# Performance work log

Measured on AMD Instinct MI355X. Metric: run time of the kernel, lower is better.

Reference implementation:

```python
import jax, jax.numpy as jnp
import numpy as np


def conv(x, w, stride=1, pad=0):
    return jax.lax.conv_general_dilated(
        x, w, (stride, stride), [(pad, pad), (pad, pad)],
        dimension_numbers=('NCHW', 'OIHW', 'NCHW'))


def group_norm(x, scale, bias, groups=32, eps=1e-5):
    B, C, H, W = x.shape
    xg = x.reshape(B, groups, C // groups, H, W)
    m = xg.mean(axis=(2, 3, 4), keepdims=True)
    v = xg.var(axis=(2, 3, 4), keepdims=True)
    xn = ((xg - m) * jax.lax.rsqrt(v + eps)).reshape(B, C, H, W)
    return xn * scale[None, :, None, None] + bias[None, :, None, None]


def bilinear_sample(x, py, px):
    # x: [B,C,H,W]; py, px: [B,K,Ho,Wo] absolute sampling coords.
    # Returns [B,C,K,Ho,Wo]; out-of-bounds corners contribute zero
    # (matches deform-conv CUDA kernel semantics).
    B, C, H, W = x.shape
    y0 = jnp.floor(py)
    x0 = jnp.floor(px)
    wy1 = py - y0
    wx1 = px - x0
    xf = x.reshape(B, C, H * W)
    Ksp = py.shape[1:]

    def corner(yi, xi, wy, wx):
        valid = (yi >= 0) & (yi < H) & (xi >= 0) & (xi < W)
        yc = jnp.clip(yi, 0, H - 1).astype(jnp.int32)
        xc = jnp.clip(xi, 0, W - 1).astype(jnp.int32)
        idx = (yc * W + xc).reshape(B, 1, -1)          # [B,1,K*Ho*Wo]
        v = jnp.take_along_axis(xf, idx, axis=2).reshape(B, C, *Ksp)
        w = (wy * wx * valid).astype(x.dtype)[:, None]  # [B,1,K,Ho,Wo]
        return v * w

    return (corner(y0, x0, 1.0 - wy1, 1.0 - wx1)
            + corner(y0, x0 + 1, 1.0 - wy1, wx1)
            + corner(y0 + 1, x0, wy1, 1.0 - wx1)
            + corner(y0 + 1, x0 + 1, wy1, wx1))


def setup_inputs() -> dict:
    key = jax.random.key(0)
    ks = jax.random.split(key, 8)
    B, Cin, H, W = 4, 1024, 64, 64
    Cb = 256  # bottleneck channels
    x = jax.random.normal(ks[0], (B, Cin, H, W), dtype=jnp.float32)
    w1 = jax.random.normal(ks[1], (Cb, Cin, 1, 1), dtype=jnp.float32) * (1.0 / np.sqrt(Cin))
    w_off = jax.random.normal(ks[2], (27, Cb, 3, 3), dtype=jnp.float32) * 0.01
    b_off = jnp.zeros((27,), dtype=jnp.float32)
    w2 = jax.random.normal(ks[3], (Cb, Cb, 3, 3), dtype=jnp.float32) * (1.0 / np.sqrt(Cb * 9))
    w3 = jax.random.normal(ks[4], (Cin, Cb, 1, 1), dtype=jnp.float32) * (1.0 / np.sqrt(Cb))
    return {
        'x': x,
        'w1': w1, 'gn1_scale': jnp.ones((Cb,), jnp.float32), 'gn1_bias': jnp.zeros((Cb,), jnp.float32),
        'w_off': w_off, 'b_off': b_off,
        'w2': w2, 'gn2_scale': jnp.ones((Cb,), jnp.float32), 'gn2_bias': jnp.zeros((Cb,), jnp.float32),
        'w3': w3, 'gn3_scale': jnp.ones((Cin,), jnp.float32), 'gn3_bias': jnp.zeros((Cin,), jnp.float32),
        'stride': 4,
    }


def reference(x, w1, gn1_scale, gn1_bias, w_off, b_off, w2, gn2_scale, gn2_bias,
              w3, gn3_scale, gn3_bias, stride):
    # stride only selects the offset-conv / norm bank (single bank here).
    out = conv(x, w1)                                   # 1x1
    out = jax.nn.relu(group_norm(out, gn1_scale, gn1_bias))

    om = conv(out, w_off, pad=1) + b_off[None, :, None, None]  # [B,27,H,W]
    K = 9
    off_x = om[:, :K]
    off_y = om[:, K:2 * K]
    mask = jax.nn.sigmoid(om[:, 2 * K:])                # [B,9,H,W]

    B, C, H, W = out.shape
    ky, kx = jnp.meshgrid(jnp.arange(3), jnp.arange(3), indexing='ij')
    ky = (ky.reshape(K) - 1).astype(om.dtype)           # kernel taps, pad=1, dil=1
    kx = (kx.reshape(K) - 1).astype(om.dtype)
    grid_y = jnp.arange(H, dtype=om.dtype)[None, :, None] + ky[:, None, None]  # [9,H,1]
    grid_x = jnp.arange(W, dtype=om.dtype)[None, None, :] + kx[:, None, None]  # [9,1,W]
    py = grid_y[None] + off_y                           # [B,9,H,W]
    px = grid_x[None] + off_x

    sampled = bilinear_sample(out, py, px) * mask[:, None]      # [B,C,9,H,W]
    out = jnp.einsum('bckhw,ock->bohw', sampled, w2.reshape(w2.shape[0], w2.shape[1], K))
    out = jax.nn.relu(group_norm(out, gn2_scale, gn2_bias))

    out = conv(out, w3)                                 # 1x1
    out = group_norm(out, gn3_scale, gn3_bias)
    return jax.nn.relu(out + x)
```

## Files before the change

kernel.cpp:

```cpp
#include <hip/hip_runtime.h>
#include <math.h>

#define BATCH 4
#define CIN   1024
#define CB    256
#define HH    64
#define WW    64
#define PP    4096
#define EPSV  1e-5f

using shortx8 = __attribute__((ext_vector_type(8))) short;
using floatx4 = __attribute__((ext_vector_type(4))) float;
using intx4   = __attribute__((ext_vector_type(4))) int;

static __device__ inline unsigned short f2bf(float f) {
    unsigned int u = __float_as_uint(f);
    u += 0x7fffu + ((u >> 16) & 1u);
    return (unsigned short)(u >> 16);
}
static __device__ inline float bf2f(unsigned short s) {
    return __uint_as_float(((unsigned int)s) << 16);
}
static __device__ inline float bflo(unsigned int u) {
    return __uint_as_float(u << 16);
}
static __device__ inline float bfhi(unsigned int u) {
    return __uint_as_float(u & 0xffff0000u);
}

__global__ __launch_bounds__(256)
void gemm_bf16(const unsigned short* __restrict__ A,
               const unsigned short* __restrict__ BTg,
               float* __restrict__ Cg, int M, int N, int K) {
    const int b = blockIdx.z;
    const unsigned short* BT = BTg + (size_t)b * N * K;
    float* C = Cg + (size_t)b * M * N;
    const int m0 = blockIdx.y * 128;
    const int n0 = blockIdx.x * 128;
    const int tid = threadIdx.x;
    const int lane = tid & 63;
    const int wid = tid >> 6;
    const int l15 = lane & 15;
    const int quad = lane >> 4;

    __shared__ __align__(16) unsigned short As[128 * 40];
    __shared__ __align__(16) unsigned short Bs[128 * 40];

    floatx4 acc[2][8];
#pragma unroll
    for (int i = 0; i < 2; i++)
#pragma unroll
        for (int j = 0; j < 8; j++) acc[i][j] = (floatx4){0.f, 0.f, 0.f, 0.f};

    const int row = tid >> 1;
    const int half = tid & 1;

    for (int k0 = 0; k0 < K; k0 += 32) {
        const unsigned short* ga = A + (size_t)(m0 + row) * K + k0 + half * 16;
        const unsigned short* gb = BT + (size_t)(n0 + row) * K + k0 + half * 16;
        float4 a0 = *(const float4*)ga;
        float4 a1 = *(const float4*)(ga + 8);
        float4 b0 = *(const float4*)gb;
        float4 b1 = *(const float4*)(gb + 8);
        __syncthreads();
        *(float4*)((char*)As + row * 80 + half * 32) = a0;
        *(float4*)((char*)As + row * 80 + half * 32 + 16) = a1;
        *(float4*)((char*)Bs + row * 80 + half * 32) = b0;
        *(float4*)((char*)Bs + row * 80 + half * 32 + 16) = b1;
        __syncthreads();
        shortx8 af[2], bf[8];
#pragma unroll
        for (int i = 0; i < 2; i++)
            af[i] = *(const shortx8*)((const char*)As +
                    (wid * 32 + 16 * i + l15) * 80 + quad * 16);
#pragma unroll
        for (int j = 0; j < 8; j++)
            bf[j] = *(const shortx8*)((const char*)Bs +
                    (16 * j + l15) * 80 + quad * 16);
#pragma unroll
        for (int i = 0; i < 2; i++)
#pragma unroll
            for (int j = 0; j < 8; j++)
                acc[i][j] = __builtin_amdgcn_mfma_f32_16x16x32_bf16(
                    af[i], bf[j], acc[i][j], 0, 0, 0);
    }

#pragma unroll
    for (int i = 0; i < 2; i++) {
#pragma unroll
        for (int r = 0; r < 4; r++) {
            int m = m0 + wid * 32 + 16 * i + quad * 4 + r;
            float* dst = C + (size_t)m * N + n0 + l15;
#pragma unroll
            for (int j = 0; j < 8; j++)
                dst[16 * j] = acc[i][j][r];
        }
    }
}

__global__ __launch_bounds__(256)
void transp_bf16(const float* __restrict__ src, unsigned short* __restrict__ dst,
                 int C, int P) {
    const int p0 = blockIdx.x * 64;
    const int c0 = blockIdx.y * 64;
    const int b = blockIdx.z;
    __shared__ unsigned short t[64][72];
    const float* s = src + ((size_t)b * C + c0) * P + p0;
    for (int e = threadIdx.x; e < 4096; e += 256) {
        int r = e >> 6, col = e & 63;
        t[r][col] = f2bf(s[(size_t)r * P + col]);
    }
    __syncthreads();
    unsigned short* d = dst + ((size_t)b * P + p0) * C + c0;
    for (int u = threadIdx.x; u < 512; u += 256) {
        int pr = u >> 3, c8 = (u & 7) * 8;
        ushort4 v0, v1;
        v0.x = t[c8 + 0][pr]; v0.y = t[c8 + 1][pr];
        v0.z = t[c8 + 2][pr]; v0.w = t[c8 + 3][pr];
        v1.x = t[c8 + 4][pr]; v1.y = t[c8 + 5][pr];
        v1.z = t[c8 + 6][pr]; v1.w = t[c8 + 7][pr];
        *(ushort4*)&d[(size_t)pr * C + c8] = v0;
        *(ushort4*)&d[(size_t)pr * C + c8 + 4] = v1;
    }
}

__global__ __launch_bounds__(256)
void gn2t(const float* __restrict__ src, const float2* __restrict__ st,
          const float* __restrict__ sc, const float* __restrict__ bi,
          unsigned short* __restrict__ dst) {
    const int p0 = blockIdx.x * 64;
    const int c0 = blockIdx.y * 64;
    const int b = blockIdx.z;
    __shared__ unsigned short t[64][72];
    const float* s = src + ((size_t)b * CB + c0) * PP + p0;
    for (int e = threadIdx.x; e < 4096; e += 256) {
        int r = e >> 6, col = e & 63;
        int c = c0 + r;
        float2 m = st[b * 32 + (c >> 3)];
        float a = m.y * sc[c];
        float bb = bi[c] - m.x * a;
        t[r][col] = f2bf(fmaxf(s[(size_t)r * PP + col] * a + bb, 0.f));
    }
    __syncthreads();
    unsigned short* d = dst + ((size_t)b * PP + p0) * CB + c0;
    for (int u = threadIdx.x; u < 512; u += 256) {
        int pr = u >> 3, c8 = (u & 7) * 8;
        ushort4 v0, v1;
        v0.x = t[c8 + 0][pr]; v0.y = t[c8 + 1][pr];
        v0.z = t[c8 + 2][pr]; v0.w = t[c8 + 3][pr];
        v1.x = t[c8 + 4][pr]; v1.y = t[c8 + 5][pr];
        v1.z = t[c8 + 6][pr]; v1.w = t[c8 + 7][pr];
        *(ushort4*)&d[(size_t)pr * CB + c8] = v0;
        *(ushort4*)&d[(size_t)pr * CB + c8 + 4] = v1;
    }
}

__global__ __launch_bounds__(256)
void gn1_dual(const float* __restrict__ src, const float2* __restrict__ st,
              const float* __restrict__ sc, const float* __restrict__ bi,
              unsigned short* __restrict__ dstC, unsigned short* __restrict__ dstT) {
    const int p0 = blockIdx.x * 64;
    const int c0 = blockIdx.y * 64;
    const int b = blockIdx.z;
    __shared__ unsigned short t[64][72];
    const float* s = src + ((size_t)b * CB + c0) * PP + p0;
    unsigned short* dc = dstC + ((size_t)b * CB + c0) * PP + p0;
    for (int e = threadIdx.x; e < 2048; e += 256) {
        int r = e >> 5, col = (e & 31) * 2;
        int c = c0 + r;
        float2 m = st[b * 32 + (c >> 3)];
        float a = m.y * sc[c];
        float bb = bi[c] - m.x * a;
        float v0 = s[(size_t)r * PP + col];
        float v1 = s[(size_t)r * PP + col + 1];
        unsigned short q0 = f2bf(fmaxf(v0 * a + bb, 0.f));
        unsigned short q1 = f2bf(fmaxf(v1 * a + bb, 0.f));
        t[r][col] = q0;
        t[r][col + 1] = q1;
        *(ushort2*)&dc[(size_t)r * PP + col] = make_ushort2(q0, q1);
    }
    __syncthreads();
    unsigned short* d = dstT + ((size_t)b * PP + p0) * CB + c0;
    for (int u = threadIdx.x; u < 512; u += 256) {
        int pr = u >> 3, c8 = (u & 7) * 8;
        ushort4 v0, v1;
        v0.x = t[c8 + 0][pr]; v0.y = t[c8 + 1][pr];
        v0.z = t[c8 + 2][pr]; v0.w = t[c8 + 3][pr];
        v1.x = t[c8 + 4][pr]; v1.y = t[c8 + 5][pr];
        v1.z = t[c8 + 6][pr]; v1.w = t[c8 + 7][pr];
        *(ushort4*)&d[(size_t)pr * CB + c8] = v0;
        *(ushort4*)&d[(size_t)pr * CB + c8 + 4] = v1;
    }
}

__global__ __launch_bounds__(256)
void cvt_bf16(const float* __restrict__ s, unsigned short* __restrict__ d, int n) {
    int i = blockIdx.x * 256 + threadIdx.x;
    if (i < n) d[i] = f2bf(s[i]);
}

__global__ __launch_bounds__(256)
void gn_stats_part(const float* __restrict__ src, float2* __restrict__ part,
                   int C, int Cpg) {
    int bgs = blockIdx.x;
    int bg = bgs >> 2, s = bgs & 3;
    int b = bg >> 5, g = bg & 31;
    const float* base = src + ((size_t)b * C + (size_t)g * Cpg) * PP;
    int n4 = (Cpg * PP) >> 2;
    int per = n4 >> 2;
    const float4* p4 = (const float4*)base + (size_t)s * per;
    float sm = 0.f, ss = 0.f;
    for (int i = threadIdx.x; i < per; i += 256) {
        float4 v = p4[i];
        sm += v.x + v.y + v.z + v.w;
        ss += v.x * v.x + v.y * v.y + v.z * v.z + v.w * v.w;
    }
    for (int off = 32; off > 0; off >>= 1) {
        sm += __shfl_down(sm, off, 64);
        ss += __shfl_down(ss, off, 64);
    }
    __shared__ float rs[4], rss[4];
    int lane = threadIdx.x & 63, wid = threadIdx.x >> 6;
    if (lane == 0) { rs[wid] = sm; rss[wid] = ss; }
    __syncthreads();
    if (threadIdx.x == 0)
        part[bgs] = make_float2(rs[0] + rs[1] + rs[2] + rs[3],
                                rss[0] + rss[1] + rss[2] + rss[3]);
}

__global__ __launch_bounds__(128)
void gn_stats_fin(const float2* __restrict__ part, float2* __restrict__ stats,
                  int cnt) {
    int bg = threadIdx.x;
    float2 p0 = part[bg * 4 + 0], p1 = part[bg * 4 + 1];
    float2 p2 = part[bg * 4 + 2], p3 = part[bg * 4 + 3];
    float S  = p0.x + p1.x + p2.x + p3.x;
    float SS = p0.y + p1.y + p2.y + p3.y;
    float mean = S / (float)cnt;
    float var = SS / (float)cnt - mean * mean;
    stats[bg] = make_float2(mean, rsqrtf(var + EPSV));
}

__global__ __launch_bounds__(256)
void om_init(float* __restrict__ om, const float* __restrict__ boff) {
    int t = blockIdx.x * 256 + threadIdx.x;
    if (t < BATCH * 27 * PP) {
        int r = (t >> 12) % 27;
        om[t] = boff[r];
    }
}

__global__ __launch_bounds__(256)
void conv_off_k(const unsigned short* __restrict__ o1bf, const float* __restrict__ w_off,
                float* __restrict__ om) {
    const int y0 = blockIdx.x * 4;
    const int c0 = blockIdx.y * 32;
    const int b = blockIdx.z;
    const int tid = threadIdx.x;
    const int tx = tid & 63, ty = tid >> 6;

    __shared__ __align__(16) float Aall[32 * 384];
    __shared__ float strip[8 * 384];

    for (int e = tid; e < 32 * 384; e += 256) {
        int c = e / 384;
        int rk = e % 384;
        int r = rk / 12, k = rk % 12;
        float v = 0.f;
        if (r < 27 && k < 9) v = w_off[((size_t)r * CB + (c0 + c)) * 9 + k];
        Aall[e] = v;
    }

    float acc[8][4];
#pragma unroll
    for (int i = 0; i < 8; i++)
#pragma unroll
        for (int j = 0; j < 4; j++) acc[i][j] = 0.f;

    for (int cg = 0; cg < 4; cg++) {
        __syncthreads();
        for (int e = tid; e < 8 * 384; e += 256) {
            int c = e / 384, rk = e % 384;
            int r = rk >> 6, col = rk & 63;
            int gy = y0 + r - 1;
            strip[e] = (gy >= 0 && gy < 64)
                ? bf2f(o1bf[(((size_t)b * CB + c0 + cg * 8 + c) << 12) + (gy << 6) + col])
                : 0.f;
        }
        __syncthreads();
        for (int c = 0; c < 8; c++) {
            float v[6][3];
#pragma unroll
            for (int r = 0; r < 6; r++)
#pragma unroll
                for (int d = 0; d < 3; d++) {
                    int col = tx + d - 1;
                    v[r][d] = (col >= 0 && col < 64) ? strip[c * 384 + r * 64 + col] : 0.f;
                }
            const float* Ac = &Aall[(cg * 8 + c) * 384];
#pragma unroll
            for (int i = 0; i < 8; i++) {
                int m = ty + 4 * i;
                float4 w0 = *(const float4*)(Ac + m * 12);
                float4 w1v = *(const float4*)(Ac + m * 12 + 4);
                float w8 = Ac[m * 12 + 8];
                float wk[9] = {w0.x, w0.y, w0.z, w0.w, w1v.x, w1v.y, w1v.z, w1v.w, w8};
#pragma unroll
                for (int kk = 0; kk < 9; kk++) {
                    int dy = kk / 3, dx = kk % 3;
#pragma unroll
                    for (int j = 0; j < 4; j++)
                        acc[i][j] += wk[kk] * v[j + dy][dx];
                }
            }
        }
    }
#pragma unroll
    for (int i = 0; i < 8; i++) {
        int m = ty + 4 * i;
        if (m < 27) {
#pragma unroll
            for (int j = 0; j < 4; j++) {
                int p = ((y0 + j) << 6) + tx;
                atomicAdd(&om[((size_t)b * 27 + m) * PP + p], acc[i][j]);
            }
        }
    }
}

__global__ __launch_bounds__(256)
void w2conv(const float* __restrict__ w2, unsigned short* __restrict__ w2bf) {
    int t = blockIdx.x * 256 + threadIdx.x;
    if (t >= 256 * 2304) return;
    int o = t / 2304;
    int r = t - o * 2304;
    int tap = r >> 8, c = r & 255;
    w2bf[t] = f2bf(w2[((size_t)o * 256 + c) * 9 + tap]);
}

__global__ __launch_bounds__(512, 2)
void gemm2_mfma(const unsigned short* __restrict__ bfAT,
                const unsigned short* __restrict__ w2bf,
                const float* __restrict__ om, float* __restrict__ out2) {
    const int blk = blockIdx.x;
    const int xcd = blk & 7;
    const int b = xcd >> 1;
    const int p0 = (((blk >> 3) << 1) | (xcd & 1)) * 64;
    const int tid = threadIdx.x;
    const int lane = tid & 63;
    const int wid = tid >> 6;
    const int l15 = lane & 15;
    const int quad = lane >> 4;

    __shared__ __align__(16) unsigned short As0[256 * 40];
    __shared__ __align__(16) unsigned short As1[256 * 40];
    __shared__ __align__(16) unsigned short Bs0[64 * 40];
    __shared__ __align__(16) unsigned short Bs1[64 * 40];
    __shared__ float sw0[576], sw1[576], sw2[576], sw3[576];
    __shared__ int   si0[576], si1[576];

    const float* ob = om + (size_t)b * 27 * PP;
    for (int e = tid; e < 576; e += 512) {
        int k = e >> 6, p = e & 63;
        int pg = p0 + p;
        float offx = ob[(size_t)k * PP + pg];
        float offy = ob[(size_t)(9 + k) * PP + pg];
        float ms = 1.f / (1.f + expf(-ob[(size_t)(18 + k) * PP + pg]));
        int y = pg >> 6, x = pg & 63;
        float py = (float)(y + k / 3 - 1) + offy;
        float px = (float)(x + (k % 3) - 1) + offx;
        float y0f = floorf(py), x0f = floorf(px);
        float wy1 = py - y0f, wx1 = px - x0f;
        int iy0 = (int)y0f, ix0 = (int)x0f;
        int iy1 = iy0 + 1;
        float wy0v = (iy0 >= 0 && iy0 < 64) ? (1.f - wy1) * ms : 0.f;
        float wy1v = (iy1 >= 0 && iy1 < 64) ? wy1 * ms : 0.f;
        int cy0 = min(max(iy0, 0), 63), cy1 = min(max(iy1, 0), 63);
        float xa, xb; int q;
        if (ix0 >= 0 && ix0 <= 62)      { q = ix0; xa = 1.f - wx1; xb = wx1;       }
        else if (ix0 == -1)             { q = 0;   xa = wx1;       xb = 0.f;       }
        else if (ix0 == 63)             { q = 62;  xa = 0.f;       xb = 1.f - wx1; }
        else                            { q = 0;   xa = 0.f;       xb = 0.f;       }
        sw0[e] = wy0v * xa;
        sw1[e] = wy0v * xb;
        sw2[e] = wy1v * xa;
        sw3[e] = wy1v * xb;
        si0[e] = (cy0 << 6) + q;
        si1[e] = (cy1 << 6) + q;
    }

    floatx4 acc[2][4];
#pragma unroll
    for (int i = 0; i < 2; i++)
#pragma unroll
        for (int j = 0; j < 4; j++) acc[i][j] = (floatx4){0.f, 0.f, 0.f, 0.f};

    const int cq = tid & 7;
    const int bp = tid >> 3;
    const int so = tid >> 1;
    const int sh = tid & 1;
    const unsigned short* xbase = bfAT + (((size_t)b) << 20);
    const unsigned short* abase = w2bf + (size_t)so * 2304 + sh * 32;
    const unsigned short* gbq = xbase + cq * 8;
    const int mbase = wid * 32;

    __syncthreads();

    float4 a0, a1, a2, a3;
    uint4 v00, v01, v10, v11;
    float w0, w1, w2v, w3v;
    {
        a0 = ((const float4*)abase)[0];
        a1 = ((const float4*)abase)[1];
        a2 = ((const float4*)abase)[2];
        a3 = ((const float4*)abase)[3];
        int tix = bp;
        w0 = sw0[tix]; w1 = sw1[tix]; w2v = sw2[tix]; w3v = sw3[tix];
        int r0 = si0[tix], r1 = si1[tix];
        v00 = *(const uint4*)(gbq + ((size_t)r0 << 8));
        v01 = *(const uint4*)(gbq + ((size_t)(r0 + 1) << 8));
        v10 = *(const uint4*)(gbq + ((size_t)r1 << 8));
        v11 = *(const uint4*)(gbq + ((size_t)(r1 + 1) << 8));
    }

    int tap = 0, cc2 = 0;
    for (int seg = 0; seg < 36; ++seg) {
        float f0 = w0 * bflo(v00.x) + w1 * bflo(v01.x)
                 + w2v * bflo(v10.x) + w3v * bflo(v11.x);
        float f1 = w0 * bfhi(v00.x) + w1 * bfhi(v01.x)
                 + w2v * bfhi(v10.x) + w3v * bfhi(v11.x);
        float f2 = w0 * bflo(v00.y) + w1 * bflo(v01.y)
                 + w2v * bflo(v10.y) + w3v * bflo(v11.y);
        float f3 = w0 * bfhi(v00.y) + w1 * bfhi(v01.y)
                 + w2v * bfhi(v10.y) + w3v * bfhi(v11.y);
        float f4 = w0 * bflo(v00.z) + w1 * bflo(v01.z)
                 + w2v * bflo(v10.z) + w3v * bflo(v11.z);
        float f5 = w0 * bfhi(v00.z) + w1 * bfhi(v01.z)
                 + w2v * bfhi(v10.z) + w3v * bfhi(v11.z);
        float f6 = w0 * bflo(v00.w) + w1 * bflo(v01.w)
                 + w2v * bflo(v10.w) + w3v * bflo(v11.w);
        float f7 = w0 * bfhi(v00.w) + w1 * bfhi(v01.w)
                 + w2v * bfhi(v10.w) + w3v * bfhi(v11.w);
        uint4 bw;
        bw.x = (unsigned int)f2bf(f0) | ((unsigned int)f2bf(f1) << 16);
        bw.y = (unsigned int)f2bf(f2) | ((unsigned int)f2bf(f3) << 16);
        bw.z = (unsigned int)f2bf(f4) | ((unsigned int)f2bf(f5) << 16);
        bw.w = (unsigned int)f2bf(f6) | ((unsigned int)f2bf(f7) << 16);
        unsigned short* adst = sh ? As1 : As0;
        *(float4*)((char*)adst + so * 80 +  0) = a0;
        *(float4*)((char*)adst + so * 80 + 16) = a1;
        *(float4*)((char*)adst + so * 80 + 32) = a2;
        *(float4*)((char*)adst + so * 80 + 48) = a3;
        unsigned short* bdst = (cq & 4) ? Bs1 : Bs0;
        *(uint4*)((char*)bdst + bp * 80 + (cq & 3) * 16) = bw;
        __syncthreads();

        int ntap = tap + 1, ncc2 = cc2;
        if (ntap == 9) { ntap = 0; ncc2 = (cc2 + 1) & 3; }
        {
            const unsigned short* gsrc = abase + ntap * 256 + ncc2 * 64;
            a0 = ((const float4*)gsrc)[0];
            a1 = ((const float4*)gsrc)[1];
            a2 = ((const float4*)gsrc)[2];
            a3 = ((const float4*)gsrc)[3];
            int tix = ntap * 64 + bp;
            int r0 = si0[tix], r1 = si1[tix];
            const unsigned short* gb = gbq + ncc2 * 64;
            v00 = *(const uint4*)(gb + ((size_t)r0 << 8));
            v01 = *(const uint4*)(gb + ((size_t)(r0 + 1) << 8));
            v10 = *(const uint4*)(gb + ((size_t)r1 << 8));
            v11 = *(const uint4*)(gb + ((size_t)(r1 + 1) << 8));
            w0 = sw0[tix]; w1 = sw1[tix]; w2v = sw2[tix]; w3v = sw3[tix];
        }

        shortx8 af[2][2], bfr[2][4];
#pragma unroll
        for (int i = 0; i < 2; i++) {
            af[0][i] = *(const shortx8*)((const char*)As0 +
                       (mbase + 16 * i + l15) * 80 + quad * 16);
            af[1][i] = *(const shortx8*)((const char*)As1 +
                       (mbase + 16 * i + l15) * 80 + quad * 16);
        }
#pragma unroll
        for (int j = 0; j < 4; j++) {
            bfr[0][j] = *(const shortx8*)((const char*)Bs0 +
                        (16 * j + l15) * 80 + quad * 16);
            bfr[1][j] = *(const shortx8*)((const char*)Bs1 +
                        (16 * j + l15) * 80 + quad * 16);
        }
#pragma unroll
        for (int ks = 0; ks < 2; ks++)
#pragma unroll
            for (int i = 0; i < 2; i++)
#pragma unroll
                for (int j = 0; j < 4; j++)
                    acc[i][j] = __builtin_amdgcn_mfma_f32_16x16x32_bf16(
                        af[ks][i], bfr[ks][j], acc[i][j], 0, 0, 0);
        __syncthreads();
        tap = ntap; cc2 = ncc2;
    }

    const size_t chbase = ((size_t)b * CB) << 12;
#pragma unroll
    for (int i = 0; i < 2; i++) {
#pragma unroll
        for (int r = 0; r < 4; r++) {
            int row = mbase + 16 * i + quad * 4 + r;
            float* dst = out2 + chbase + ((size_t)row << 12) + p0 + l15;
#pragma unroll
            for (int j = 0; j < 4; j++)
                dst[16 * j] = acc[i][j][r];
        }
    }
}

__global__ __launch_bounds__(256)
void final_k(float* __restrict__ dout, const float* __restrict__ x,
             const float2* __restrict__ stats, const float* __restrict__ sc,
             const float* __restrict__ bi) {
    long i = (long)blockIdx.x * 256 + threadIdx.x;
    long total4 = ((long)BATCH * CIN * PP) >> 2;
    if (i >= total4) return;
    long e = i << 2;
    int c = (int)((e >> 12) & 1023);
    int b = (int)(e >> 22);
    float2 st = stats[b * 32 + (c >> 5)];
    float a = st.y * sc[c];
    float bb = bi[c] - st.x * a;
    float4 v = ((float4*)dout)[i];
    float4 xv = ((const float4*)x)[i];
    v.x = fmaxf(v.x * a + bb + xv.x, 0.f);
    v.y = fmaxf(v.y * a + bb + xv.y, 0.f);
    v.z = fmaxf(v.z * a + bb + xv.z, 0.f);
    v.w = fmaxf(v.w * a + bb + xv.w, 0.f);
    ((float4*)dout)[i] = v;
}

extern "C" void kernel_launch(void* const* d_in, const int* in_sizes, int n_in,
                              void* d_out, int out_size, void* d_ws, size_t ws_size,
                              hipStream_t stream) {
    const float* x   = (const float*)d_in[0];
    const float* w1  = (const float*)d_in[1];
    const float* g1s = (const float*)d_in[2];
    const float* g1b = (const float*)d_in[3];
    const float* wof = (const float*)d_in[4];
    const float* bof = (const float*)d_in[5];
    const float* w2  = (const float*)d_in[6];
    const float* g2s = (const float*)d_in[7];
    const float* g2b = (const float*)d_in[8];
    const float* w3  = (const float*)d_in[9];
    const float* g3s = (const float*)d_in[10];
    const float* g3b = (const float*)d_in[11];
    float* out = (float*)d_out;

    float* ws = (float*)d_ws;
    unsigned short* w1bf   = (unsigned short*)(ws + 0);
    float*          out1r  = ws + 131072;
    float*          out2   = ws + 131072;
    unsigned short* xbfT   = (unsigned short*)(ws + 4325376);
    unsigned short* bfA    = (unsigned short*)(ws + 4325376);
    unsigned short* bfAT   = (unsigned short*)(ws + 6422528);
    float*          om     = ws + 8519680;
    unsigned short* w2bf   = (unsigned short*)(ws + 8962048);
    unsigned short* out2bT = (unsigned short*)(ws + 4325376);
    unsigned short* w3bf   = (unsigned short*)(ws + 11354112);
    float2* st1  = (float2*)(ws + 11485184);
    float2* st2  = st1 + 128;
    float2* st3  = st2 + 128;
    float2* part = st3 + 128;

    transp_bf16<<<dim3(64, 16, 4), 256, 0, stream>>>(x, xbfT, 1024, 4096);
    cvt_bf16<<<1024, 256, 0, stream>>>(w1, w1bf, 262144);
    gemm_bf16<<<dim3(32, 2, 4), 256, 0, stream>>>(w1bf, xbfT, out1r, 256, 4096, 1024);
    gn_stats_part<<<512, 256, 0, stream>>>(out1r, part, 256, 8);
    gn_stats_fin<<<1, 128, 0, stream>>>(part, st1, 8 * PP);
    gn1_dual<<<dim3(64, 4, 4), 256, 0, stream>>>(out1r, st1, g1s, g1b, bfA, bfAT);
    om_init<<<1728, 256, 0, stream>>>(om, bof);
    conv_off_k<<<dim3(16, 8, 4), 256, 0, stream>>>(bfA, wof, om);
    w2conv<<<2304, 256, 0, stream>>>(w2, w2bf);
    cvt_bf16<<<1024, 256, 0, stream>>>(w3, w3bf, 262144);
    gemm2_mfma<<<dim3(256, 1, 1), 512, 0, stream>>>(bfAT, w2bf, om, out2);
    gn_stats_part<<<512, 256, 0, stream>>>(out2, part, 256, 8);
    gn_stats_fin<<<1, 128, 0, stream>>>(part, st2, 8 * PP);
    gn2t<<<dim3(64, 4, 4), 256, 0, stream>>>(out2, st2, g2s, g2b, out2bT);
    gemm_bf16<<<dim3(32, 8, 4), 256, 0, stream>>>(w3bf, out2bT, out, 1024, 4096, 256);
    gn_stats_part<<<512, 256, 0, stream>>>(out, part, 1024, 32);
    gn_stats_fin<<<1, 128, 0, stream>>>(part, st3, 32 * PP);
    final_k<<<16384, 256, 0, stream>>>(out, x, st3, g3s, g3b);
}
```

Baseline: 386.4 us.

## Compute offset conv with bf16 MFMA on channel-last activations

Replaces the scalar FP32 offset/mask 3x3 convolution, which used atomics and a separate bias-init kernel, with an MFMA implicit-GEMM over the transposed bf16 activations. A new kernel reorders the offset weights to bf16 with a [m][tap][c] layout padded to 32 rows. The bias is added in the epilogue and there are no atomics. Because the channel-major bf16 copy is no longer needed, gn1_dual is replaced with gn2t, which writes only the transposed output. Computing the offset weights in bf16 may change offset precision slightly.

Result: faster. 348.8 us (-9.7%).

```diff
diff --git a/kernel.cpp b/kernel.cpp
--- a/kernel.cpp
+++ b/kernel.cpp
@@ -156,44 +156,6 @@
 }
 
 __global__ __launch_bounds__(256)
-void gn1_dual(const float* __restrict__ src, const float2* __restrict__ st,
-              const float* __restrict__ sc, const float* __restrict__ bi,
-              unsigned short* __restrict__ dstC, unsigned short* __restrict__ dstT) {
-    const int p0 = blockIdx.x * 64;
-    const int c0 = blockIdx.y * 64;
-    const int b = blockIdx.z;
-    __shared__ unsigned short t[64][72];
-    const float* s = src + ((size_t)b * CB + c0) * PP + p0;
-    unsigned short* dc = dstC + ((size_t)b * CB + c0) * PP + p0;
-    for (int e = threadIdx.x; e < 2048; e += 256) {
-        int r = e >> 5, col = (e & 31) * 2;
-        int c = c0 + r;
-        float2 m = st[b * 32 + (c >> 3)];
-        float a = m.y * sc[c];
-        float bb = bi[c] - m.x * a;
-        float v0 = s[(size_t)r * PP + col];
-        float v1 = s[(size_t)r * PP + col + 1];
-        unsigned short q0 = f2bf(fmaxf(v0 * a + bb, 0.f));
-        unsigned short q1 = f2bf(fmaxf(v1 * a + bb, 0.f));
-        t[r][col] = q0;
-        t[r][col + 1] = q1;
-        *(ushort2*)&dc[(size_t)r * PP + col] = make_ushort2(q0, q1);
-    }
-    __syncthreads();
-    unsigned short* d = dstT + ((size_t)b * PP + p0) * CB + c0;
-    for (int u = threadIdx.x; u < 512; u += 256) {
-        int pr = u >> 3, c8 = (u & 7) * 8;
-        ushort4 v0, v1;
-        v0.x = t[c8 + 0][pr]; v0.y = t[c8 + 1][pr];
-        v0.z = t[c8 + 2][pr]; v0.w = t[c8 + 3][pr];
-        v1.x = t[c8 + 4][pr]; v1.y = t[c8 + 5][pr];
-        v1.z = t[c8 + 6][pr]; v1.w = t[c8 + 7][pr];
-        *(ushort4*)&d[(size_t)pr * CB + c8] = v0;
-        *(ushort4*)&d[(size_t)pr * CB + c8 + 4] = v1;
-    }
-}
-
-__global__ __launch_bounds__(256)
 void cvt_bf16(const float* __restrict__ s, unsigned short* __restrict__ d, int n) {
     int i = blockIdx.x * 256 + threadIdx.x;
     if (i < n) d[i] = f2bf(s[i]);
@@ -242,100 +204,75 @@
 }
 
 __global__ __launch_bounds__(256)
-void om_init(float* __restrict__ om, const float* __restrict__ boff) {
+void woff_conv(const float* __restrict__ w_off, unsigned short* __restrict__ wobf) {
     int t = blockIdx.x * 256 + threadIdx.x;
-    if (t < BATCH * 27 * PP) {
-        int r = (t >> 12) % 27;
-        om[t] = boff[r];
-    }
-}
-
-__global__ __launch_bounds__(256)
-void conv_off_k(const unsigned short* __restrict__ o1bf, const float* __restrict__ w_off,
-                float* __restrict__ om) {
-    const int y0 = blockIdx.x * 4;
-    const int c0 = blockIdx.y * 32;
-    const int b = blockIdx.z;
+    if (t >= 32 * 2304) return;
+    int m = t / 2304;
+    int r = t - m * 2304;
+    int tap = r >> 8, c = r & 255;
+    float v = (m < 27) ? w_off[((size_t)m * 256 + c) * 9 + tap] : 0.f;
+    wobf[t] = f2bf(v);
+}
+
+__global__ __launch_bounds__(256)
+void conv_off_mfma(const unsigned short* __restrict__ bfAT,
+                   const unsigned short* __restrict__ wobf,
+                   const float* __restrict__ boff,
+                   float* __restrict__ om) {
+    const int blk = blockIdx.x;
+    const int xcd = blk & 7;
+    const int b = xcd >> 1;
+    const int tile = ((blk >> 3) << 1) | (xcd & 1);
+    const int p0 = tile * 32;
     const int tid = threadIdx.x;
-    const int tx = tid & 63, ty = tid >> 6;
-
-    __shared__ __align__(16) float Aall[32 * 384];
-    __shared__ float strip[8 * 384];
-
-    for (int e = tid; e < 32 * 384; e += 256) {
-        int c = e / 384;
-        int rk = e % 384;
-        int r = rk / 12, k = rk % 12;
-        float v = 0.f;
-        if (r < 27 && k < 9) v = w_off[((size_t)r * CB + (c0 + c)) * 9 + k];
-        Aall[e] = v;
-    }
-
-    float acc[8][4];
-#pragma unroll
-    for (int i = 0; i < 8; i++)
-#pragma unroll
-        for (int j = 0; j < 4; j++) acc[i][j] = 0.f;
-
-    for (int cg = 0; cg < 4; cg++) {
+    const int lane = tid & 63;
+    const int wid = tid >> 6;
+    const int l15 = lane & 15;
+    const int quad = lane >> 4;
+    const int mh = (wid >> 1) << 4;
+    const int ph = (wid & 1) << 4;
+
+    __shared__ __align__(16) unsigned short Bs[8 * 1288];
+
+    const int y0r = p0 >> 6;
+    const int x0 = p0 & 63;
+    const unsigned short* xb = bfAT + ((size_t)b << 20);
+    const unsigned short* arow = wobf + (size_t)(mh + l15) * 2304 + quad * 8;
+
+    floatx4 acc = (floatx4){0.f, 0.f, 0.f, 0.f};
+
+    for (int tap = 0; tap < 9; ++tap) {
+        const int dy = tap / 3 - 1, dx = tap % 3 - 1;
+        const int yy = y0r + dy;
+        const bool rowok = (yy >= 0 && yy < 64);
         __syncthreads();
-        for (int e = tid; e < 8 * 384; e += 256) {
-            int c = e / 384, rk = e % 384;
-            int r = rk >> 6, col = rk & 63;
-            int gy = y0 + r - 1;
-            strip[e] = (gy >= 0 && gy < 64)
-                ? bf2f(o1bf[(((size_t)b * CB + c0 + cg * 8 + c) << 12) + (gy << 6) + col])
-                : 0.f;
+        for (int e = tid; e < 1024; e += 256) {
+            int px = e >> 5, ck = e & 31;
+            int xx = x0 + px + dx;
+            uint4 v = make_uint4(0u, 0u, 0u, 0u);
+            if (rowok && xx >= 0 && xx < 64) {
+                int srow = (yy << 6) + xx;
+                v = *(const uint4*)(xb + ((size_t)srow << 8) + ck * 8);
+            }
+            *(uint4*)((char*)Bs + (ck >> 2) * 2576 + px * 80 + (ck & 3) * 16) = v;
         }
         __syncthreads();
-        for (int c = 0; c < 8; c++) {
-            float v[6][3];
-#pragma unroll
-            for (int r = 0; r < 6; r++)
-#pragma unroll
-                for (int d = 0; d < 3; d++) {
-                    int col = tx + d - 1;
-                    v[r][d] = (col >= 0 && col < 64) ? strip[c * 384 + r * 64 + col] : 0.f;
-                }
-            const float* Ac = &Aall[(cg * 8 + c) * 384];
-#pragma unroll
-            for (int i = 0; i < 8; i++) {
-                int m = ty + 4 * i;
-                float4 w0 = *(const float4*)(Ac + m * 12);
-                float4 w1v = *(const float4*)(Ac + m * 12 + 4);
-                float w8 = Ac[m * 12 + 8];
-                float wk[9] = {w0.x, w0.y, w0.z, w0.w, w1v.x, w1v.y, w1v.z, w1v.w, w8};
-#pragma unroll
-                for (int kk = 0; kk < 9; kk++) {
-                    int dy = kk / 3, dx = kk % 3;
-#pragma unroll
-                    for (int j = 0; j < 4; j++)
-                        acc[i][j] += wk[kk] * v[j + dy][dx];
-                }
-            }
-        }
-    }
-#pragma unroll
-    for (int i = 0; i < 8; i++) {
-        int m = ty + 4 * i;
-        if (m < 27) {
-#pragma unroll
-            for (int j = 0; j < 4; j++) {
-                int p = ((y0 + j) << 6) + tx;
-                atomicAdd(&om[((size_t)b * 27 + m) * PP + p], acc[i][j]);
-            }
-        }
-    }
-}
-
-__global__ __launch_bounds__(256)
-void w2conv(const float* __restrict__ w2, unsigned short* __restrict__ w2bf) {
-    int t = blockIdx.x * 256 + threadIdx.x;
-    if (t >= 256 * 2304) return;
-    int o = t / 2304;
-    int r = t - o * 2304;
-    int tap = r >> 8, c = r & 255;
-    w2bf[t] = f2bf(w2[((size_t)o * 256 + c) * 9 + tap]);
+        const unsigned short* at = arow + tap * 256;
+#pragma unroll
+        for (int cc = 0; cc < 8; ++cc) {
+            shortx8 af = *(const shortx8*)(at + cc * 32);
+            shortx8 bf = *(const shortx8*)((const char*)Bs + cc * 2576 +
+                         (ph + l15) * 80 + quad * 16);
+            acc = __builtin_amdgcn_mfma_f32_16x16x32_bf16(af, bf, acc, 0, 0, 0);
+        }
+    }
+
+#pragma unroll
+    for (int r = 0; r < 4; ++r) {
+        int m = mh + quad * 4 + r;
+        if (m < 27)
+            om[((size_t)b * 27 + m) * PP + p0 + ph + l15] = acc[r] + boff[m];
+    }
 }
 
 __global__ __launch_bounds__(512, 2)
@@ -515,6 +452,16 @@
 }
 
 __global__ __launch_bounds__(256)
+void w2conv(const float* __restrict__ w2, unsigned short* __restrict__ w2bf) {
+    int t = blockIdx.x * 256 + threadIdx.x;
+    if (t >= 256 * 2304) return;
+    int o = t / 2304;
+    int r = t - o * 2304;
+    int tap = r >> 8, c = r & 255;
+    w2bf[t] = f2bf(w2[((size_t)o * 256 + c) * 9 + tap]);
+}
+
+__global__ __launch_bounds__(256)
 void final_k(float* __restrict__ dout, const float* __restrict__ x,
              const float2* __restrict__ stats, const float* __restrict__ sc,
              const float* __restrict__ bi) {
@@ -558,10 +505,10 @@
     float*          out1r  = ws + 131072;
     float*          out2   = ws + 131072;
     unsigned short* xbfT   = (unsigned short*)(ws + 4325376);
-    unsigned short* bfA    = (unsigned short*)(ws + 4325376);
     unsigned short* bfAT   = (unsigned short*)(ws + 6422528);
     float*          om     = ws + 8519680;
     unsigned short* w2bf   = (unsigned short*)(ws + 8962048);
+    unsigned short* wobf   = (unsigned short*)(ws + 9256960);
     unsigned short* out2bT = (unsigned short*)(ws + 4325376);
     unsigned short* w3bf   = (unsigned short*)(ws + 11354112);
     float2* st1  = (float2*)(ws + 11485184);
@@ -574,9 +521,9 @@
     gemm_bf16<<<dim3(32, 2, 4), 256, 0, stream>>>(w1bf, xbfT, out1r, 256, 4096, 1024);
     gn_stats_part<<<512, 256, 0, stream>>>(out1r, part, 256, 8);
     gn_stats_fin<<<1, 128, 0, stream>>>(part, st1, 8 * PP);
-    gn1_dual<<<dim3(64, 4, 4), 256, 0, stream>>>(out1r, st1, g1s, g1b, bfA, bfAT);
-    om_init<<<1728, 256, 0, stream>>>(om, bof);
-    conv_off_k<<<dim3(16, 8, 4), 256, 0, stream>>>(bfA, wof, om);
+    gn2t<<<dim3(64, 4, 4), 256, 0, stream>>>(out1r, st1, g1s, g1b, bfAT);
+    woff_conv<<<288, 256, 0, stream>>>(wof, wobf);
+    conv_off_mfma<<<512, 256, 0, stream>>>(bfAT, wobf, bof, om);
     w2conv<<<2304, 256, 0, stream>>>(w2, w2bf);
     cvt_bf16<<<1024, 256, 0, stream>>>(w3, w3bf, 262144);
     gemm2_mfma<<<dim3(256, 1, 1), 512, 0, stream>>>(bfAT, w2bf, om, out2);
```
